# Performance work log

Measured on AMD Instinct MI355X. Metric: run time of the kernel, lower is better.

Reference implementation:

```python
import jax, jax.numpy as jnp
import numpy as np

B, N, C = 128, 196, 2048   # batch, regions (14x14), conv channels
H, A = 512, 512            # hidden_size, attention_size


def setup_inputs() -> dict:
    key = jax.random.key(0)
    ks = jax.random.split(key, 10)
    s = lambda d: 1.0 / np.sqrt(d)
    return {
        "img_embedding": jax.random.normal(ks[0], (B, N, C), jnp.float32),
        "hidden": jax.random.normal(ks[1], (B, H), jnp.float32),
        "W_img": jax.random.uniform(ks[2], (C, A), jnp.float32, -s(C), s(C)),
        "b_img": jax.random.uniform(ks[3], (A,), jnp.float32, -s(C), s(C)),
        "W_hid": jax.random.uniform(ks[4], (H, A), jnp.float32, -s(H), s(H)),
        "b_hid": jax.random.uniform(ks[5], (A,), jnp.float32, -s(H), s(H)),
        "w_att": jax.random.uniform(ks[6], (A,), jnp.float32, -s(A), s(A)),
        "b_att": jax.random.uniform(ks[7], (), jnp.float32, -s(A), s(A)),
        "w_beta": jax.random.uniform(ks[8], (H,), jnp.float32, -s(H), s(H)),
        "b_beta": jax.random.uniform(ks[9], (), jnp.float32, -s(H), s(H)),
    }


def reference(img_embedding, hidden, W_img, b_img, W_hid, b_hid,
              w_att, b_att, w_beta, b_beta):
    # img_embedding: (B, N, C); hidden: (B, H)
    img_att = jnp.einsum('bnc,ca->bna', img_embedding, W_img) + b_img   # (B,N,A)
    hid_att = hidden @ W_hid + b_hid                                    # (B,A)
    # additive attention scores -> (B, N)
    scores = jnp.einsum('bna,a->bn',
                        jax.nn.relu(img_att + hid_att[:, None, :]), w_att) + b_att
    beta = jax.nn.sigmoid(hidden @ w_beta + b_beta)                     # (B,)
    attention_weights = jax.nn.softmax(scores, axis=-1)                 # (B,N)
    context = beta[:, None] * jnp.einsum('bn,bnc->bc',
                                         attention_weights, img_embedding)  # (B,C)
    return context, attention_weights
```

## Files before the change

kernel.cpp:

```cpp
#include <hip/hip_runtime.h>
#include <hip/hip_bf16.h>
#include <math.h>

typedef __bf16 bf16v8 __attribute__((ext_vector_type(8)));
typedef float  f32x4  __attribute__((ext_vector_type(4)));

__device__ __forceinline__ void gload_lds16(const void* g, void* l) {
    __builtin_amdgcn_global_load_lds(
        (const __attribute__((address_space(1))) unsigned int*)g,
        (__attribute__((address_space(3))) unsigned int*)l, 16, 0, 0);
}

__device__ __forceinline__ void cvt_store8(void* dst, float4 a, float4 b) {
    bf16v8 v;
    v[0] = (__bf16)a.x; v[1] = (__bf16)a.y; v[2] = (__bf16)a.z; v[3] = (__bf16)a.w;
    v[4] = (__bf16)b.x; v[5] = (__bf16)b.y; v[6] = (__bf16)b.z; v[7] = (__bf16)b.w;
    *(bf16v8*)dst = v;
}

__global__ __launch_bounds__(256) void wt_k(const float* __restrict__ W,
                                            unsigned short* __restrict__ Wt)
{
    __shared__ float tile[64][65];
    const int k0 = blockIdx.x * 64;
    const int a0 = blockIdx.y * 64;
    const int t = threadIdx.x;
    const int c = t & 63, rbase = t >> 6;
#pragma unroll
    for (int i = 0; i < 16; ++i) {
        int kr = rbase + i * 4;
        tile[kr][c] = W[(k0 + kr) * 512 + a0 + c];
    }
    __syncthreads();
#pragma unroll
    for (int i = 0; i < 16; ++i) {
        int ar = rbase + i * 4;
        Wt[(a0 + ar) * 2048 + k0 + c] =
            __builtin_bit_cast(unsigned short, (__bf16)tile[c][ar]);
    }
}

__global__ __launch_bounds__(256) void hid_k(
    const float* __restrict__ hidden, const float* __restrict__ W_hid,
    const float* __restrict__ b_hid,  const float* __restrict__ b_img,
    const float* __restrict__ w_beta, const float* __restrict__ b_beta,
    float* __restrict__ hb, float* __restrict__ betap)
{
    const int b = blockIdx.x, t = threadIdx.x;
    __shared__ float hs[512];
    __shared__ float red[4];
    hs[t]       = hidden[b * 512 + t];
    hs[t + 256] = hidden[b * 512 + 256 + t];
    __syncthreads();
    float a0 = 0.f, a1 = 0.f;
#pragma unroll 4
    for (int h = 0; h < 512; ++h) {
        float hv = hs[h];
        a0 = fmaf(hv, W_hid[h * 512 + t], a0);
        a1 = fmaf(hv, W_hid[h * 512 + 256 + t], a1);
    }
    hb[b * 512 + t]       = a0 + b_hid[t]       + b_img[t];
    hb[b * 512 + 256 + t] = a1 + b_hid[256 + t] + b_img[256 + t];

    float x = hs[t] * w_beta[t] + hs[t + 256] * w_beta[t + 256];
#pragma unroll
    for (int k = 32; k >= 1; k >>= 1) x += __shfl_xor(x, k, 64);
    const int lane = t & 63, wid = t >> 6;
    if (lane == 0) red[wid] = x;
    __syncthreads();
    if (t == 0) {
        float s = red[0] + red[1] + red[2] + red[3] + b_beta[0];
        betap[b] = 1.f / (1.f + __expf(-s));
    }
}

#define NKIT 64

__global__ __launch_bounds__(256, 4) void scores_gemm(
    const float* __restrict__ img,
    const unsigned short* __restrict__ Wt,
    const float* __restrict__ hb,
    const float* __restrict__ w_att,
    float* __restrict__ partials)
{
    __shared__ __align__(16) char smem[26624];
    char* A0 = smem;
    char* A1 = smem + 5120;
    char* B0 = smem + 10240;
    char* B1 = smem + 18432;

    const int tid  = threadIdx.x;
    const int lane = tid & 63;
    const int wid  = tid >> 6;
    const int wm   = wid >> 1;
    const int wn   = wid & 1;

    const int id = blockIdx.x;
    const int wg = (id & 7) * 196 + (id >> 3);
    const int cb    = wg & 3;
    const int mtile = wg >> 2;
    const int r0 = mtile * 64;
    const int a0 = cb * 128;

    const int arow = tid >> 2;
    const int aq   = tid & 3;
    const float* gA = img + (size_t)(r0 + arow) * 2048 + aq * 8;
    const int aW = arow * 80 + aq * 16;

    const int bswz = ((tid & 3) ^ ((tid >> 3) & 3)) * 8;
    const unsigned short* gB0 = Wt + (size_t)(a0 + (tid >> 2)) * 2048 + bswz;
    const unsigned short* gB1 = Wt + (size_t)(a0 + 64 + (tid >> 2)) * 2048 + bswz;
    const int bW0 = tid * 16;
    const int bW1 = 4096 + tid * 16;

    const int g  = lane >> 4;
    const int fl = lane & 15;
    const int bro = (g ^ ((fl >> 1) & 3)) << 4;

    f32x4 acc[2][4] = {};
    float4 rA0[2], rA1[2];

    rA0[0] = *(const float4*)(gA);
    rA0[1] = *(const float4*)(gA + 4);
    gload_lds16(gB0, B0 + bW0);
    gload_lds16(gB1, B0 + bW1);
    __builtin_amdgcn_sched_barrier(0);
    cvt_store8(A0 + aW, rA0[0], rA0[1]);
    rA0[0] = *(const float4*)(gA + 32);
    rA0[1] = *(const float4*)(gA + 36);
    rA1[0] = *(const float4*)(gA + 64);
    rA1[1] = *(const float4*)(gA + 68);
    __syncthreads();

#define BODY(K, CA, CB, NA, NB, RC, STAGE, RELOAD, FULLBAR) do {            \
    bf16v8 av0, av1, bv0, bv1, bv2, bv3;                                     \
    {                                                                        \
        int row0 = wm * 32 + fl;                                             \
        av0 = *(const bf16v8*)(CA + row0 * 80 + g * 16);                     \
        av1 = *(const bf16v8*)(CA + (row0 + 16) * 80 + g * 16);              \
        int c0 = wn * 64 + fl;                                               \
        bv0 = *(const bf16v8*)(CB + c0 * 64 + bro);                          \
        bv1 = *(const bf16v8*)(CB + (c0 + 16) * 64 + bro);                   \
        bv2 = *(const bf16v8*)(CB + (c0 + 32) * 64 + bro);                   \
        bv3 = *(const bf16v8*)(CB + (c0 + 48) * 64 + bro);                   \
    }                                                                        \
    if (STAGE) {                                                             \
        gload_lds16(gB0 + (K + 1) * 32, NB + bW0);                           \
        gload_lds16(gB1 + (K + 1) * 32, NB + bW1);                           \
    }                                                                        \
    __builtin_amdgcn_sched_barrier(0);                                       \
    if (STAGE) cvt_store8(NA + aW, RC[0], RC[1]);                            \
    if (RELOAD) {                                                            \
        RC[0] = *(const float4*)(gA + (K + 3) * 32);                         \
        RC[1] = *(const float4*)(gA + (K + 3) * 32 + 4);                     \
    }                                                                        \
    __builtin_amdgcn_sched_barrier(0);                                       \
    acc[0][0] = __builtin_amdgcn_mfma_f32_16x16x32_bf16(av0, bv0, acc[0][0], 0, 0, 0); \
    acc[0][1] = __builtin_amdgcn_mfma_f32_16x16x32_bf16(av0, bv1, acc[0][1], 0, 0, 0); \
    acc[0][2] = __builtin_amdgcn_mfma_f32_16x16x32_bf16(av0, bv2, acc[0][2], 0, 0, 0); \
    acc[0][3] = __builtin_amdgcn_mfma_f32_16x16x32_bf16(av0, bv3, acc[0][3], 0, 0, 0); \
    acc[1][0] = __builtin_amdgcn_mfma_f32_16x16x32_bf16(av1, bv0, acc[1][0], 0, 0, 0); \
    acc[1][1] = __builtin_amdgcn_mfma_f32_16x16x32_bf16(av1, bv1, acc[1][1], 0, 0, 0); \
    acc[1][2] = __builtin_amdgcn_mfma_f32_16x16x32_bf16(av1, bv2, acc[1][2], 0, 0, 0); \
    acc[1][3] = __builtin_amdgcn_mfma_f32_16x16x32_bf16(av1, bv3, acc[1][3], 0, 0, 0); \
    if (FULLBAR) {                                                           \
        __syncthreads();                                                     \
    } else {                                                                 \
        __builtin_amdgcn_sched_barrier(0);                                   \
        asm volatile("s_waitcnt vmcnt(2) lgkmcnt(0)" ::: "memory");          \
        __builtin_amdgcn_s_barrier();                                        \
        __builtin_amdgcn_sched_barrier(0);                                   \
    }                                                                        \
} while (0)

    for (int t = 0; t < 60; t += 2) {
        BODY(t,     A0, B0, A1, B1, rA0, true, true, false);
        BODY(t + 1, A1, B1, A0, B0, rA1, true, true, false);
    }
    BODY(60, A0, B0, A1, B1, rA0, true,  true,  true);
    BODY(61, A1, B1, A0, B0, rA1, true,  false, true);
    BODY(62, A0, B0, A1, B1, rA0, true,  false, true);
    BODY(63, A1, B1, A0, B0, rA1, false, false, true);
#undef BODY

    float* red = (float*)smem;
    const int l4 = lane >> 4;

    float w4[4];
#pragma unroll
    for (int fn = 0; fn < 4; ++fn) w4[fn] = w_att[a0 + wn * 64 + fn * 16 + fl];

#pragma unroll
    for (int fm = 0; fm < 2; ++fm) {
#pragma unroll
        for (int rg = 0; rg < 4; ++rg) {
            int row = wm * 32 + fm * 16 + l4 * 4 + rg;
            int grow = r0 + row;
            int bb = grow / 196;
            const float* hbrow = hb + bb * 512 + a0 + wn * 64;
            float s = 0.f;
#pragma unroll
            for (int fn = 0; fn < 4; ++fn) {
                float v = acc[fm][fn][rg] + hbrow[fn * 16 + fl];
                v = fmaxf(v, 0.f);
                s = fmaf(v, w4[fn], s);
            }
#pragma unroll
            for (int m = 1; m < 16; m <<= 1) s += __shfl_xor(s, m, 64);
            if (fl == 0) red[wn * 64 + row] = s;
        }
    }
    __syncthreads();
    if (tid < 64) {
        partials[cb * 25088 + r0 + tid] = red[tid] + red[64 + tid];
    }
}

__global__ __launch_bounds__(256) void softmax_k(
    const float* __restrict__ partials, const float* __restrict__ betap,
    const float* __restrict__ b_att,
    float* __restrict__ out_w, float* __restrict__ wbeta)
{
    const int b = blockIdx.x;
    const int t = threadIdx.x;
    const int lane = t & 63, wid = t >> 6;
    __shared__ float red[4];

    float scv = 0.f, sc = -1e30f;
    if (t < 196) {
        int r = b * 196 + t;
        scv = partials[r] + partials[25088 + r] + partials[2 * 25088 + r] +
              partials[3 * 25088 + r] + b_att[0];
        sc = scv;
    }
    float m = sc;
#pragma unroll
    for (int k = 32; k >= 1; k >>= 1) m = fmaxf(m, __shfl_xor(m, k, 64));
    if (lane == 0) red[wid] = m;
    __syncthreads();
    m = fmaxf(fmaxf(red[0], red[1]), fmaxf(red[2], red[3]));

    float e = (t < 196) ? __expf(scv - m) : 0.f;
    float ssum = e;
#pragma unroll
    for (int k = 32; k >= 1; k >>= 1) ssum += __shfl_xor(ssum, k, 64);
    __syncthreads();
    if (lane == 0) red[wid] = ssum;
    __syncthreads();
    float denom = red[0] + red[1] + red[2] + red[3];

    if (t < 196) {
        float w = e / denom;
        out_w[b * 196 + t] = w;
        wbeta[b * 196 + t] = w * betap[b];
    }
}

__global__ __launch_bounds__(256) void ctx_k(
    const float* __restrict__ img, const float* __restrict__ wbeta,
    float* __restrict__ out)
{
    const int b = blockIdx.y;
    const int c0 = blockIdx.x * 512 + threadIdx.x * 2;
    __shared__ float w[200];
    if (threadIdx.x < 196) w[threadIdx.x] = wbeta[b * 196 + threadIdx.x];
    __syncthreads();
    const float* base = img + (size_t)b * 196 * 2048 + c0;
    float acx = 0.f, acy = 0.f;
#pragma unroll 4
    for (int n = 0; n < 196; ++n) {
        float2 v = *(const float2*)(base + (size_t)n * 2048);
        float wn = w[n];
        acx = fmaf(wn, v.x, acx);
        acy = fmaf(wn, v.y, acy);
    }
    float2 r; r.x = acx; r.y = acy;
    *(float2*)(out + b * 2048 + c0) = r;
}

extern "C" void kernel_launch(void* const* d_in, const int* in_sizes, int n_in,
                              void* d_out, int out_size, void* d_ws, size_t ws_size,
                              hipStream_t stream)
{
    const float* img    = (const float*)d_in[0];
    const float* hidden = (const float*)d_in[1];
    const float* W_img  = (const float*)d_in[2];
    const float* b_img  = (const float*)d_in[3];
    const float* W_hid  = (const float*)d_in[4];
    const float* b_hid  = (const float*)d_in[5];
    const float* w_att  = (const float*)d_in[6];
    const float* b_att  = (const float*)d_in[7];
    const float* w_beta = (const float*)d_in[8];
    const float* b_beta = (const float*)d_in[9];

    char* ws = (char*)d_ws;
    unsigned short* Wt = (unsigned short*)ws;
    float* hbp   = (float*)(ws + 2097152);
    float* betap = (float*)(ws + 2359296);
    float* parts = (float*)(ws + 2359808);
    float* wbeta = (float*)(ws + 2761216);

    float* out_ctx = (float*)d_out;
    float* out_w   = out_ctx + 128 * 2048;

    wt_k<<<dim3(32, 8), 256, 0, stream>>>(W_img, Wt);
    hid_k<<<128, 256, 0, stream>>>(hidden, W_hid, b_hid, b_img, w_beta, b_beta,
                                   hbp, betap);
    scores_gemm<<<1568, 256, 0, stream>>>(img, Wt, hbp, w_att, parts);
    softmax_k<<<128, 256, 0, stream>>>(parts, betap, b_att, out_w, wbeta);
    ctx_k<<<dim3(4, 128), 256, 0, stream>>>(img, wbeta, out_ctx);
}
```

Measured before the change: 180.1 us.

## Triple-buffer W tiles in LDS to prefetch two k-steps ahead

Moves the bf16 weight-tile staging in the scores GEMM from double to triple buffering, so global-to-LDS loads for B are issued two iterations ahead instead of one. The wait count is relaxed so more loads stay in flight across the per-iteration barrier, and the main loop is unrolled by six to rotate the three B buffers. The aim is to hide more global load latency. In exchange, LDS per block grows from 26 KB to 34 KB, which can reduce how many blocks fit per CU.

After: 184.2 us. 2.3% more time.

```diff
diff --git a/kernel.cpp b/kernel.cpp
--- a/kernel.cpp
+++ b/kernel.cpp
@@ -83,11 +83,12 @@
     const float* __restrict__ w_att,
     float* __restrict__ partials)
 {
-    __shared__ __align__(16) char smem[26624];
-    char* A0 = smem;
-    char* A1 = smem + 5120;
-    char* B0 = smem + 10240;
-    char* B1 = smem + 18432;
+    __shared__ __align__(16) char smem[34816];
+    char* A0  = smem;
+    char* A1  = smem + 5120;
+    char* Bb0 = smem + 10240;
+    char* Bb1 = smem + 18432;
+    char* Bb2 = smem + 26624;
 
     const int tid  = threadIdx.x;
     const int lane = tid & 63;
@@ -122,8 +123,10 @@
 
     rA0[0] = *(const float4*)(gA);
     rA0[1] = *(const float4*)(gA + 4);
-    gload_lds16(gB0, B0 + bW0);
-    gload_lds16(gB1, B0 + bW1);
+    gload_lds16(gB0, Bb0 + bW0);
+    gload_lds16(gB1, Bb0 + bW1);
+    gload_lds16(gB0 + 32, Bb1 + bW0);
+    gload_lds16(gB1 + 32, Bb1 + bW1);
     __builtin_amdgcn_sched_barrier(0);
     cvt_store8(A0 + aW, rA0[0], rA0[1]);
     rA0[0] = *(const float4*)(gA + 32);
@@ -132,7 +135,7 @@
     rA1[1] = *(const float4*)(gA + 68);
     __syncthreads();
 
-#define BODY(K, CA, CB, NA, NB, RC, STAGE, RELOAD, FULLBAR) do {            \
+#define BODY(K, CA, CB, NB, NA, RC, STAGEB, DOCVT, RELOAD, FULLBAR) do {    \
     bf16v8 av0, av1, bv0, bv1, bv2, bv3;                                     \
     {                                                                        \
         int row0 = wm * 32 + fl;                                             \
@@ -144,12 +147,12 @@
         bv2 = *(const bf16v8*)(CB + (c0 + 32) * 64 + bro);                   \
         bv3 = *(const bf16v8*)(CB + (c0 + 48) * 64 + bro);                   \
     }                                                                        \
-    if (STAGE) {                                                             \
-        gload_lds16(gB0 + (K + 1) * 32, NB + bW0);                           \
-        gload_lds16(gB1 + (K + 1) * 32, NB + bW1);                           \
+    if (STAGEB) {                                                            \
+        gload_lds16(gB0 + (K + 2) * 32, NB + bW0);                           \
+        gload_lds16(gB1 + (K + 2) * 32, NB + bW1);                           \
     }                                                                        \
     __builtin_amdgcn_sched_barrier(0);                                       \
-    if (STAGE) cvt_store8(NA + aW, RC[0], RC[1]);                            \
+    if (DOCVT) cvt_store8(NA + aW, RC[0], RC[1]);                            \
     if (RELOAD) {                                                            \
         RC[0] = *(const float4*)(gA + (K + 3) * 32);                         \
         RC[1] = *(const float4*)(gA + (K + 3) * 32 + 4);                     \
@@ -167,20 +170,24 @@
         __syncthreads();                                                     \
     } else {                                                                 \
         __builtin_amdgcn_sched_barrier(0);                                   \
-        asm volatile("s_waitcnt vmcnt(2) lgkmcnt(0)" ::: "memory");          \
+        asm volatile("s_waitcnt vmcnt(6) lgkmcnt(0)" ::: "memory");          \
         __builtin_amdgcn_s_barrier();                                        \
         __builtin_amdgcn_sched_barrier(0);                                   \
     }                                                                        \
 } while (0)
 
-    for (int t = 0; t < 60; t += 2) {
-        BODY(t,     A0, B0, A1, B1, rA0, true, true, false);
-        BODY(t + 1, A1, B1, A0, B0, rA1, true, true, false);
-    }
-    BODY(60, A0, B0, A1, B1, rA0, true,  true,  true);
-    BODY(61, A1, B1, A0, B0, rA1, true,  false, true);
-    BODY(62, A0, B0, A1, B1, rA0, true,  false, true);
-    BODY(63, A1, B1, A0, B0, rA1, false, false, true);
+    for (int t = 0; t < 60; t += 6) {
+        BODY(t,     A0, Bb0, Bb2, A1, rA0, true, true, true, false);
+        BODY(t + 1, A1, Bb1, Bb0, A0, rA1, true, true, true, false);
+        BODY(t + 2, A0, Bb2, Bb1, A1, rA0, true, true, true, false);
+        BODY(t + 3, A1, Bb0, Bb2, A0, rA1, true, true, true, false);
+        BODY(t + 4, A0, Bb1, Bb0, A1, rA0, true, true, true, false);
+        BODY(t + 5, A1, Bb2, Bb1, A0, rA1, true, true, true, false);
+    }
+    BODY(60, A0, Bb0, Bb2, A1, rA0, true,  true,  true,  false);
+    BODY(61, A1, Bb1, Bb0, A0, rA1, true,  true,  false, true);
+    BODY(62, A0, Bb2, Bb1, A1, rA0, false, true,  false, true);
+    BODY(63, A1, Bb0, Bb2, A0, rA1, false, false, false, true);
 #undef BODY
 
     float* red = (float*)smem;
```

## Enlarge scores GEMM tile to 128 rows per workgroup with 4x4 MFMA fragments

Applied to the files above, without the earlier changes.

The scores GEMM block tile grows from 64x128 to 128x128. Each wave now computes a 64x64 sub-tile with a 4x4 grid of MFMA accumulators, and the grid shrinks from 1568 to 784 workgroups. The goal is to halve how often the converted W_img (B operand) tiles are reloaded per image row and to raise MFMA work per LDS read. In exchange the kernel uses more LDS and registers, occupancy drops to 3 blocks per SIMD set, the A-load pattern and waitcnt depth change, and fewer blocks are available to fill the GPU.

Result: slower. 210.9 us (+17.1%).

```diff
diff --git a/kernel.cpp b/kernel.cpp
--- a/kernel.cpp
+++ b/kernel.cpp
@@ -3,6 +3,7 @@
 #include <math.h>
 
 typedef __bf16 bf16v8 __attribute__((ext_vector_type(8)));
+typedef __bf16 bf16v4 __attribute__((ext_vector_type(4)));
 typedef float  f32x4  __attribute__((ext_vector_type(4)));
 
 __device__ __forceinline__ void gload_lds16(const void* g, void* l) {
@@ -11,11 +12,11 @@
         (__attribute__((address_space(3))) unsigned int*)l, 16, 0, 0);
 }
 
-__device__ __forceinline__ void cvt_store8(void* dst, float4 a, float4 b) {
-    bf16v8 v;
-    v[0] = (__bf16)a.x; v[1] = (__bf16)a.y; v[2] = (__bf16)a.z; v[3] = (__bf16)a.w;
-    v[4] = (__bf16)b.x; v[5] = (__bf16)b.y; v[6] = (__bf16)b.z; v[7] = (__bf16)b.w;
-    *(bf16v8*)dst = v;
+__device__ __forceinline__ void cvt_w4(void* dst, float4 a) {
+    bf16v4 v;
+    v[0] = (__bf16)a.x; v[1] = (__bf16)a.y;
+    v[2] = (__bf16)a.z; v[3] = (__bf16)a.w;
+    *(bf16v4*)dst = v;
 }
 
 __global__ __launch_bounds__(256) void wt_k(const float* __restrict__ W,
@@ -74,20 +75,18 @@
     }
 }
 
-#define NKIT 64
-
-__global__ __launch_bounds__(256, 4) void scores_gemm(
+__global__ __launch_bounds__(256, 3) void scores_gemm(
     const float* __restrict__ img,
     const unsigned short* __restrict__ Wt,
     const float* __restrict__ hb,
     const float* __restrict__ w_att,
     float* __restrict__ partials)
 {
-    __shared__ __align__(16) char smem[26624];
+    __shared__ __align__(16) char smem[36864];
     char* A0 = smem;
-    char* A1 = smem + 5120;
-    char* B0 = smem + 10240;
-    char* B1 = smem + 18432;
+    char* A1 = smem + 10240;
+    char* B0 = smem + 20480;
+    char* B1 = smem + 28672;
 
     const int tid  = threadIdx.x;
     const int lane = tid & 63;
@@ -96,16 +95,18 @@
     const int wn   = wid & 1;
 
     const int id = blockIdx.x;
-    const int wg = (id & 7) * 196 + (id >> 3);
+    const int wg = (id & 7) * 98 + (id >> 3);
     const int cb    = wg & 3;
     const int mtile = wg >> 2;
-    const int r0 = mtile * 64;
+    const int r0 = mtile * 128;
     const int a0 = cb * 128;
 
-    const int arow = tid >> 2;
-    const int aq   = tid & 3;
-    const float* gA = img + (size_t)(r0 + arow) * 2048 + aq * 8;
-    const int aW = arow * 80 + aq * 16;
+    const int ar = tid >> 2;
+    const int ac = (tid & 3) * 4;
+    const float* gA0 = img + (size_t)(r0 + ar) * 2048 + ac;
+    const float* gA1 = img + (size_t)(r0 + 64 + ar) * 2048 + ac;
+    const int aW0 = ar * 80 + ac * 2;
+    const int aW1 = (64 + ar) * 80 + ac * 2;
 
     const int bswz = ((tid & 3) ^ ((tid >> 3) & 3)) * 8;
     const unsigned short* gB0 = Wt + (size_t)(a0 + (tid >> 2)) * 2048 + bswz;
@@ -117,57 +118,63 @@
     const int fl = lane & 15;
     const int bro = (g ^ ((fl >> 1) & 3)) << 4;
 
-    f32x4 acc[2][4] = {};
-    float4 rA0[2], rA1[2];
-
-    rA0[0] = *(const float4*)(gA);
-    rA0[1] = *(const float4*)(gA + 4);
+    f32x4 acc[4][4] = {};
+    float4 rA0[4], rA1[4];
+
+#define ALOAD(RC, IT) do {                                                   \
+    RC[0] = *(const float4*)(gA0 + (IT) * 32);                               \
+    RC[1] = *(const float4*)(gA0 + (IT) * 32 + 16);                          \
+    RC[2] = *(const float4*)(gA1 + (IT) * 32);                               \
+    RC[3] = *(const float4*)(gA1 + (IT) * 32 + 16);                          \
+} while (0)
+
+#define ACVT(DST, RC) do {                                                   \
+    cvt_w4(DST + aW0,      RC[0]);                                           \
+    cvt_w4(DST + aW0 + 32, RC[1]);                                           \
+    cvt_w4(DST + aW1,      RC[2]);                                           \
+    cvt_w4(DST + aW1 + 32, RC[3]);                                           \
+} while (0)
+
+    ALOAD(rA0, 0);
     gload_lds16(gB0, B0 + bW0);
     gload_lds16(gB1, B0 + bW1);
     __builtin_amdgcn_sched_barrier(0);
-    cvt_store8(A0 + aW, rA0[0], rA0[1]);
-    rA0[0] = *(const float4*)(gA + 32);
-    rA0[1] = *(const float4*)(gA + 36);
-    rA1[0] = *(const float4*)(gA + 64);
-    rA1[1] = *(const float4*)(gA + 68);
-    __syncthreads();
-
-#define BODY(K, CA, CB, NA, NB, RC, STAGE, RELOAD, FULLBAR) do {            \
-    bf16v8 av0, av1, bv0, bv1, bv2, bv3;                                     \
-    {                                                                        \
-        int row0 = wm * 32 + fl;                                             \
-        av0 = *(const bf16v8*)(CA + row0 * 80 + g * 16);                     \
-        av1 = *(const bf16v8*)(CA + (row0 + 16) * 80 + g * 16);              \
-        int c0 = wn * 64 + fl;                                               \
-        bv0 = *(const bf16v8*)(CB + c0 * 64 + bro);                          \
-        bv1 = *(const bf16v8*)(CB + (c0 + 16) * 64 + bro);                   \
-        bv2 = *(const bf16v8*)(CB + (c0 + 32) * 64 + bro);                   \
-        bv3 = *(const bf16v8*)(CB + (c0 + 48) * 64 + bro);                   \
+    ACVT(A0, rA0);
+    ALOAD(rA0, 1);
+    ALOAD(rA1, 2);
+    __syncthreads();
+
+#define BODY(K, CA, CB, NA, NB, RC, STAGE, RELOAD, FULLBAR) do {             \
+    bf16v8 av[4], bv[4];                                                     \
+    _Pragma("unroll")                                                        \
+    for (int fm = 0; fm < 4; ++fm) {                                         \
+        int row = wm * 64 + fm * 16 + fl;                                    \
+        av[fm] = *(const bf16v8*)(CA + row * 80 + g * 16);                   \
+    }                                                                        \
+    _Pragma("unroll")                                                        \
+    for (int fn = 0; fn < 4; ++fn) {                                         \
+        int col = wn * 64 + fn * 16 + fl;                                    \
+        bv[fn] = *(const bf16v8*)(CB + col * 64 + bro);                      \
     }                                                                        \
     if (STAGE) {                                                             \
         gload_lds16(gB0 + (K + 1) * 32, NB + bW0);                           \
         gload_lds16(gB1 + (K + 1) * 32, NB + bW1);                           \
     }                                                                        \
     __builtin_amdgcn_sched_barrier(0);                                       \
-    if (STAGE) cvt_store8(NA + aW, RC[0], RC[1]);                            \
-    if (RELOAD) {                                                            \
-        RC[0] = *(const float4*)(gA + (K + 3) * 32);                         \
-        RC[1] = *(const float4*)(gA + (K + 3) * 32 + 4);                     \
-    }                                                                        \
+    if (STAGE) ACVT(NA, RC);                                                 \
+    if (RELOAD) ALOAD(RC, K + 3);                                            \
     __builtin_amdgcn_sched_barrier(0);                                       \
-    acc[0][0] = __builtin_amdgcn_mfma_f32_16x16x32_bf16(av0, bv0, acc[0][0], 0, 0, 0); \
-    acc[0][1] = __builtin_amdgcn_mfma_f32_16x16x32_bf16(av0, bv1, acc[0][1], 0, 0, 0); \
-    acc[0][2] = __builtin_amdgcn_mfma_f32_16x16x32_bf16(av0, bv2, acc[0][2], 0, 0, 0); \
-    acc[0][3] = __builtin_amdgcn_mfma_f32_16x16x32_bf16(av0, bv3, acc[0][3], 0, 0, 0); \
-    acc[1][0] = __builtin_amdgcn_mfma_f32_16x16x32_bf16(av1, bv0, acc[1][0], 0, 0, 0); \
-    acc[1][1] = __builtin_amdgcn_mfma_f32_16x16x32_bf16(av1, bv1, acc[1][1], 0, 0, 0); \
-    acc[1][2] = __builtin_amdgcn_mfma_f32_16x16x32_bf16(av1, bv2, acc[1][2], 0, 0, 0); \
-    acc[1][3] = __builtin_amdgcn_mfma_f32_16x16x32_bf16(av1, bv3, acc[1][3], 0, 0, 0); \
+    _Pragma("unroll")                                                        \
+    for (int fm = 0; fm < 4; ++fm)                                           \
+        _Pragma("unroll")                                                    \
+        for (int fn = 0; fn < 4; ++fn)                                       \
+            acc[fm][fn] = __builtin_amdgcn_mfma_f32_16x16x32_bf16(           \
+                av[fm], bv[fn], acc[fm][fn], 0, 0, 0);                       \
     if (FULLBAR) {                                                           \
         __syncthreads();                                                     \
     } else {                                                                 \
         __builtin_amdgcn_sched_barrier(0);                                   \
-        asm volatile("s_waitcnt vmcnt(2) lgkmcnt(0)" ::: "memory");          \
+        asm volatile("s_waitcnt vmcnt(4) lgkmcnt(0)" ::: "memory");          \
         __builtin_amdgcn_s_barrier();                                        \
         __builtin_amdgcn_sched_barrier(0);                                   \
     }                                                                        \
@@ -177,11 +184,13 @@
         BODY(t,     A0, B0, A1, B1, rA0, true, true, false);
         BODY(t + 1, A1, B1, A0, B0, rA1, true, true, false);
     }
-    BODY(60, A0, B0, A1, B1, rA0, true,  true,  true);
+    BODY(60, A0, B0, A1, B1, rA0, true,  true,  false);
     BODY(61, A1, B1, A0, B0, rA1, true,  false, true);
     BODY(62, A0, B0, A1, B1, rA0, true,  false, true);
     BODY(63, A1, B1, A0, B0, rA1, false, false, true);
 #undef BODY
+#undef ALOAD
+#undef ACVT
 
     float* red = (float*)smem;
     const int l4 = lane >> 4;
@@ -191,10 +200,10 @@
     for (int fn = 0; fn < 4; ++fn) w4[fn] = w_att[a0 + wn * 64 + fn * 16 + fl];
 
 #pragma unroll
-    for (int fm = 0; fm < 2; ++fm) {
+    for (int fm = 0; fm < 4; ++fm) {
 #pragma unroll
         for (int rg = 0; rg < 4; ++rg) {
-            int row = wm * 32 + fm * 16 + l4 * 4 + rg;
+            int row = wm * 64 + fm * 16 + l4 * 4 + rg;
             int grow = r0 + row;
             int bb = grow / 196;
             const float* hbrow = hb + bb * 512 + a0 + wn * 64;
@@ -207,12 +216,12 @@
             }
 #pragma unroll
             for (int m = 1; m < 16; m <<= 1) s += __shfl_xor(s, m, 64);
-            if (fl == 0) red[wn * 64 + row] = s;
+            if (fl == 0) red[wn * 128 + row] = s;
         }
     }
     __syncthreads();
-    if (tid < 64) {
-        partials[cb * 25088 + r0 + tid] = red[tid] + red[64 + tid];
+    if (tid < 128) {
+        partials[cb * 25088 + r0 + tid] = red[tid] + red[128 + tid];
     }
 }
 
@@ -306,7 +315,7 @@
     wt_k<<<dim3(32, 8), 256, 0, stream>>>(W_img, Wt);
     hid_k<<<128, 256, 0, stream>>>(hidden, W_hid, b_hid, b_img, w_beta, b_beta,
                                    hbp, betap);
-    scores_gemm<<<1568, 256, 0, stream>>>(img, Wt, hbp, w_att, parts);
+    scores_gemm<<<784, 256, 0, stream>>>(img, Wt, hbp, w_att, parts);
     softmax_k<<<128, 256, 0, stream>>>(parts, betap, b_att, out_w, wbeta);
     ctx_k<<<dim3(4, 128), 256, 0, stream>>>(img, wbeta, out_ctx);
 }
```
